# Kernel tuning notes

Measured on AMD Instinct MI355X. Metric: run time of the kernel, lower is better.

The kernel has to match this reference:

```python
import jax, jax.numpy as jnp
import numpy as np

EPS = 0.1

def setup_inputs() -> dict:
    key = jax.random.key(0)
    k1, k2, k3, k4, k5, k6 = jax.random.split(key, 6)
    B, N, Cin, Cout = 8, 2048, 128, 128
    x = jax.random.normal(k1, (B, N, Cin), dtype=jnp.float32)
    x_0 = jax.random.normal(k2, (B, N, Cout), dtype=jnp.float32)
    adj = jax.random.randint(k3, (B, N, N), 0, 2, dtype=jnp.int32)
    # learned parameters (Linear without bias stores weight [out,in]; we keep [in,out])
    W_lin = jax.random.normal(k4, (Cin, Cout), dtype=jnp.float32) / np.sqrt(Cin)
    w_att_l = jax.random.normal(k5, (Cout,), dtype=jnp.float32) / np.sqrt(Cout)
    w_att_r = jax.random.normal(k6, (Cout,), dtype=jnp.float32) / np.sqrt(Cout)
    return {"x": x, "x_0": x_0, "adj": adj, "W_lin": W_lin, "w_att_l": w_att_l, "w_att_r": w_att_r}

def reference(x, x_0, adj, W_lin, w_att_l, w_att_r):
    # x: [B,N,Cin] -> h: [B,N,Cout]
    h = jnp.einsum('bni,io->bno', x, W_lin)
    alpha_l = jnp.einsum('bno,o->bn', h, w_att_l)  # [B,N]
    alpha_r = jnp.einsum('bno,o->bn', h, w_att_r)  # [B,N]
    # alpha[b,i,j] = tanh(alpha_r[b,i] * alpha_l[b,j])
    alpha = jnp.tanh(alpha_r[:, :, None] * alpha_l[:, None, :])  # [B,N,N]
    alpha = jnp.where(adj == 0, jnp.float32(0.0), alpha)
    # dropout p=0.0 -> identity
    out = jnp.einsum('bij,bjo->bio', alpha, h)  # [B,N,Cout]
    return out + EPS * x_0
```

## Files before the change

### kernel.cpp

```cpp
#include <hip/hip_runtime.h>
#include <stdint.h>

#define B_   8
#define N_   2048
#define C_   128
#define EPS_ 0.1f

typedef __attribute__((ext_vector_type(8))) short short8;
typedef __attribute__((ext_vector_type(4))) float f32x4;

__device__ __forceinline__ unsigned short f2bf(float f) {
    union { float f; uint32_t u; } v; v.f = f;
    uint32_t u = v.u + 0x7FFF + ((v.u >> 16) & 1);
    return (unsigned short)(u >> 16);
}

__global__ __launch_bounds__(128) void k_wt(const float* __restrict__ W,
                                            unsigned short* __restrict__ Wt) {
    const int o = blockIdx.x, k = threadIdx.x;
    Wt[o * C_ + k] = f2bf(W[k * C_ + o]);
}

__global__ __launch_bounds__(256) void k_h(
    const float* __restrict__ x, const unsigned short* __restrict__ Wt,
    const float* __restrict__ wl, const float* __restrict__ wr,
    unsigned short* __restrict__ ht, float* __restrict__ al, float* __restrict__ ar)
{
    const int b    = blockIdx.x >> 5;
    const int i0   = (blockIdx.x & 31) * 64;
    const int t    = threadIdx.x;
    const int lane = t & 63;
    const int wid  = t >> 6;

    __shared__ __align__(16) unsigned short xs[64 * 128];
    __shared__ __align__(16) unsigned short ws[128 * 128];

    #pragma unroll
    for (int p = 0; p < 4; ++p) {
        const int s = p * 256 + t, row = s >> 4, u = s & 15;
        const float* gp = x + ((size_t)(b * N_ + i0 + row) * C_ + u * 8);
        float4 f0 = *(const float4*)gp;
        float4 f1 = *(const float4*)(gp + 4);
        short8 tv;
        tv[0] = (short)f2bf(f0.x); tv[1] = (short)f2bf(f0.y);
        tv[2] = (short)f2bf(f0.z); tv[3] = (short)f2bf(f0.w);
        tv[4] = (short)f2bf(f1.x); tv[5] = (short)f2bf(f1.y);
        tv[6] = (short)f2bf(f1.z); tv[7] = (short)f2bf(f1.w);
        *(short8*)&xs[row * 128 + (u ^ (row & 15)) * 8] = tv;
    }
    #pragma unroll
    for (int p = 0; p < 8; ++p) {
        const int s = p * 256 + t, o = s >> 4, u = s & 15;
        int4 v = *(const int4*)(Wt + o * C_ + u * 8);
        *(int4*)&ws[o * 128 + (u ^ (o & 15)) * 8] = v;
    }
    __syncthreads();

    const int m0 = wid * 16, lr = lane & 15, q = lane >> 4;
    f32x4 acc[8];
    #pragma unroll
    for (int i = 0; i < 8; ++i) acc[i] = (f32x4){0.f, 0.f, 0.f, 0.f};

    #pragma unroll
    for (int s = 0; s < 4; ++s) {
        const int m = m0 + lr;
        short8 af = *(const short8*)&xs[m * 128 + ((s * 4 + q) ^ (m & 15)) * 8];
        #pragma unroll
        for (int tt = 0; tt < 8; ++tt) {
            const int o = tt * 16 + lr;
            short8 bf = *(const short8*)&ws[o * 128 + ((s * 4 + q) ^ (o & 15)) * 8];
            acc[tt] = __builtin_amdgcn_mfma_f32_16x16x32_bf16(af, bf, acc[tt], 0, 0, 0);
        }
    }

    float pl[4] = {0.f, 0.f, 0.f, 0.f}, pr[4] = {0.f, 0.f, 0.f, 0.f};
    const int j0 = i0 + m0 + q * 4;
    #pragma unroll
    for (int tt = 0; tt < 8; ++tt) {
        const int o = tt * 16 + lr;
        const float wlv = wl[o], wrv = wr[o];
        unsigned int lo = (unsigned int)f2bf(acc[tt][0]) | ((unsigned int)f2bf(acc[tt][1]) << 16);
        unsigned int hi = (unsigned int)f2bf(acc[tt][2]) | ((unsigned int)f2bf(acc[tt][3]) << 16);
        uint2 u2; u2.x = lo; u2.y = hi;
        *(uint2*)&ht[((size_t)(b * C_ + o)) * N_ + j0] = u2;
        #pragma unroll
        for (int r = 0; r < 4; ++r) {
            pl[r] = fmaf(acc[tt][r], wlv, pl[r]);
            pr[r] = fmaf(acc[tt][r], wrv, pr[r]);
        }
    }
    #pragma unroll
    for (int msk = 1; msk < 16; msk <<= 1) {
        #pragma unroll
        for (int r = 0; r < 4; ++r) {
            pl[r] += __shfl_xor(pl[r], msk, 64);
            pr[r] += __shfl_xor(pr[r], msk, 64);
        }
    }
    if (lr == 0) {
        #pragma unroll
        for (int r = 0; r < 4; ++r) {
            al[b * N_ + j0 + r] = pl[r];
            ar[b * N_ + j0 + r] = pr[r];
        }
    }
}

struct Pref {
    int4   a[4];
    float4 l[4];
    int4   hb[8];
};

__global__ __launch_bounds__(256) void k_out(
    const int* __restrict__ adj, const unsigned short* __restrict__ ht,
    const float* __restrict__ al, const float* __restrict__ ar,
    const float* __restrict__ x0, float* __restrict__ out)
{
    const int b    = blockIdx.x >> 6;
    const int i0   = (blockIdx.x & 63) * 32;
    const int t    = threadIdx.x;
    const int lane = t & 63;
    const int wid  = t >> 6;

    const int m0 = (wid & 1) * 16, n0 = (wid >> 1) * 64;
    const int lr = lane & 15, q = lane >> 4;
    const int q8 = q * 8;

    const int irow = i0 + m0 + lr;
    const float arv = ar[b * N_ + irow];
    const float tl  = 2.f * arv;
    const int*            adjp = adj + ((size_t)(b * N_) + irow) * N_;
    const float*          alp  = al + b * N_;
    const unsigned short* hbp  = ht + ((size_t)(b * C_) + n0 + lr) * N_;

    auto ldc = [&](int c) -> Pref {
        Pref P;
        const int j0 = c * 64 + q8;
        #pragma unroll
        for (int s2 = 0; s2 < 2; ++s2) {
            P.a[s2 * 2]     = *(const int4*)(adjp + j0 + s2 * 32);
            P.a[s2 * 2 + 1] = *(const int4*)(adjp + j0 + s2 * 32 + 4);
            P.l[s2 * 2]     = *(const float4*)(alp + j0 + s2 * 32);
            P.l[s2 * 2 + 1] = *(const float4*)(alp + j0 + s2 * 32 + 4);
            #pragma unroll
            for (int tt = 0; tt < 4; ++tt)
                P.hb[s2 * 4 + tt] =
                    *(const int4*)(hbp + (size_t)(tt * 16) * N_ + j0 + s2 * 32);
        }
        return P;
    };

    f32x4 acc[4];
    #pragma unroll
    for (int i = 0; i < 4; ++i) acc[i] = (f32x4){0.f, 0.f, 0.f, 0.f};

    auto cmp = [&](const Pref& P) {
        #pragma unroll
        for (int s2 = 0; s2 < 2; ++s2) {
            const int*   av = (const int*)&P.a[s2 * 2];
            const float* lv = (const float*)&P.l[s2 * 2];
            short8 af;
            #pragma unroll
            for (int e = 0; e < 8; ++e) {
                float ex = __expf(tl * lv[e]);
                float th = 1.f - 2.f / (ex + 1.f);
                af[e] = av[e] ? (short)f2bf(th) : (short)0;
            }
            #pragma unroll
            for (int tt = 0; tt < 4; ++tt) {
                short8 bf = *(const short8*)&P.hb[s2 * 4 + tt];
                acc[tt] = __builtin_amdgcn_mfma_f32_16x16x32_bf16(af, bf, acc[tt], 0, 0, 0);
            }
        }
    };

    Pref PA = ldc(0);
    #pragma unroll 1
    for (int c = 0; c < 32; c += 2) {
        Pref PB = ldc(c + 1);
        cmp(PA);
        if (c + 2 < 32) PA = ldc(c + 2);
        cmp(PB);
    }

    #pragma unroll
    for (int tt = 0; tt < 4; ++tt) {
        const int o = n0 + tt * 16 + lr;
        #pragma unroll
        for (int r = 0; r < 4; ++r) {
            const int row = i0 + m0 + q * 4 + r;
            const size_t idx = ((size_t)(b * N_) + row) * C_ + o;
            out[idx] = acc[tt][r] + EPS_ * x0[idx];
        }
    }
}

extern "C" void kernel_launch(void* const* d_in, const int* in_sizes, int n_in,
                              void* d_out, int out_size, void* d_ws, size_t ws_size,
                              hipStream_t stream) {
    const float* x   = (const float*)d_in[0];
    const float* x0  = (const float*)d_in[1];
    const int*   adj = (const int*)d_in[2];
    const float* W   = (const float*)d_in[3];
    const float* wl  = (const float*)d_in[4];
    const float* wr  = (const float*)d_in[5];
    float* out = (float*)d_out;

    unsigned short* ht = (unsigned short*)d_ws;
    float* al = (float*)((char*)d_ws + (size_t)B_ * C_ * N_ * 2);
    float* ar = al + B_ * N_;
    unsigned short* Wt = (unsigned short*)(ar + B_ * N_);

    k_wt <<<C_,             C_,  0, stream>>>(W, Wt);
    k_h  <<<B_ * (N_ / 64), 256, 0, stream>>>(x, Wt, wl, wr, ht, al, ar);
    k_out<<<B_ * (N_ / 32), 256, 0, stream>>>(adj, ht, al, ar, x0, out);
}
```

Before: 270.3 us.

## Split k_out over the reduction dimension with LDS cross-wave sum

```diff
diff --git a/kernel.cpp b/kernel.cpp
--- a/kernel.cpp
+++ b/kernel.cpp
@@ -106,94 +106,89 @@
     }
 }
 
-struct Pref {
-    int4   a[4];
-    float4 l[4];
-    int4   hb[8];
-};
-
 __global__ __launch_bounds__(256) void k_out(
     const int* __restrict__ adj, const unsigned short* __restrict__ ht,
     const float* __restrict__ al, const float* __restrict__ ar,
     const float* __restrict__ x0, float* __restrict__ out)
 {
-    const int b    = blockIdx.x >> 6;
-    const int i0   = (blockIdx.x & 63) * 32;
+    const int b    = blockIdx.x & 7;
+    const int i0   = (blockIdx.x >> 3) * 16;
     const int t    = threadIdx.x;
     const int lane = t & 63;
     const int wid  = t >> 6;
-
-    const int m0 = (wid & 1) * 16, n0 = (wid >> 1) * 64;
-    const int lr = lane & 15, q = lane >> 4;
-    const int q8 = q * 8;
-
-    const int irow = i0 + m0 + lr;
-    const float arv = ar[b * N_ + irow];
+    const int lr   = lane & 15, q = lane >> 4;
+
+    __shared__ __align__(16) float red[4][16][132];
+
+    const float arv = ar[b * N_ + i0 + lr];
     const float tl  = 2.f * arv;
-    const int*            adjp = adj + ((size_t)(b * N_) + irow) * N_;
-    const float*          alp  = al + b * N_;
-    const unsigned short* hbp  = ht + ((size_t)(b * C_) + n0 + lr) * N_;
-
-    auto ldc = [&](int c) -> Pref {
-        Pref P;
-        const int j0 = c * 64 + q8;
+
+    const int*            adjp = adj + ((size_t)(b * N_) + i0 + lr) * N_ + q * 8;
+    const float*          alp  = al + b * N_ + q * 8;
+    const unsigned short* htp  = ht + ((size_t)(b * C_) + lr) * N_ + q * 8;
+
+    f32x4 acc[8];
+    #pragma unroll
+    for (int i = 0; i < 8; ++i) acc[i] = (f32x4){0.f, 0.f, 0.f, 0.f};
+
+    #pragma unroll 1
+    for (int k = 0; k < 8; ++k) {
+        const int j0 = (wid * 8 + k) * 64;
         #pragma unroll
         for (int s2 = 0; s2 < 2; ++s2) {
-            P.a[s2 * 2]     = *(const int4*)(adjp + j0 + s2 * 32);
-            P.a[s2 * 2 + 1] = *(const int4*)(adjp + j0 + s2 * 32 + 4);
-            P.l[s2 * 2]     = *(const float4*)(alp + j0 + s2 * 32);
-            P.l[s2 * 2 + 1] = *(const float4*)(alp + j0 + s2 * 32 + 4);
-            #pragma unroll
-            for (int tt = 0; tt < 4; ++tt)
-                P.hb[s2 * 4 + tt] =
-                    *(const int4*)(hbp + (size_t)(tt * 16) * N_ + j0 + s2 * 32);
-        }
-        return P;
-    };
-
-    f32x4 acc[4];
-    #pragma unroll
-    for (int i = 0; i < 4; ++i) acc[i] = (f32x4){0.f, 0.f, 0.f, 0.f};
-
-    auto cmp = [&](const Pref& P) {
-        #pragma unroll
-        for (int s2 = 0; s2 < 2; ++s2) {
-            const int*   av = (const int*)&P.a[s2 * 2];
-            const float* lv = (const float*)&P.l[s2 * 2];
+            const int jo = j0 + s2 * 32;
+            int4 a01[2];
+            a01[0] = *(const int4*)(adjp + jo);
+            a01[1] = *(const int4*)(adjp + jo + 4);
+            float4 l01[2];
+            l01[0] = *(const float4*)(alp + jo);
+            l01[1] = *(const float4*)(alp + jo + 4);
+            const int*   av = (const int*)a01;
+            const float* lv = (const float*)l01;
             short8 af;
             #pragma unroll
             for (int e = 0; e < 8; ++e) {
                 float ex = __expf(tl * lv[e]);
-                float th = 1.f - 2.f / (ex + 1.f);
+                float th = 1.f - 2.f * __builtin_amdgcn_rcpf(ex + 1.f);
                 af[e] = av[e] ? (short)f2bf(th) : (short)0;
             }
             #pragma unroll
-            for (int tt = 0; tt < 4; ++tt) {
-                short8 bf = *(const short8*)&P.hb[s2 * 4 + tt];
+            for (int tt = 0; tt < 8; ++tt) {
+                short8 bf = *(const short8*)(htp + (size_t)(tt * 16) * N_ + jo);
                 acc[tt] = __builtin_amdgcn_mfma_f32_16x16x32_bf16(af, bf, acc[tt], 0, 0, 0);
             }
         }
-    };
-
-    Pref PA = ldc(0);
-    #pragma unroll 1
-    for (int c = 0; c < 32; c += 2) {
-        Pref PB = ldc(c + 1);
-        cmp(PA);
-        if (c + 2 < 32) PA = ldc(c + 2);
-        cmp(PB);
-    }
-
-    #pragma unroll
-    for (int tt = 0; tt < 4; ++tt) {
-        const int o = n0 + tt * 16 + lr;
-        #pragma unroll
-        for (int r = 0; r < 4; ++r) {
-            const int row = i0 + m0 + q * 4 + r;
-            const size_t idx = ((size_t)(b * N_) + row) * C_ + o;
-            out[idx] = acc[tt][r] + EPS_ * x0[idx];
-        }
-    }
+    }
+
+    #pragma unroll
+    for (int tt = 0; tt < 8; ++tt)
+        #pragma unroll
+        for (int r = 0; r < 4; ++r)
+            red[wid][q * 4 + r][tt * 16 + lr] = acc[tt][r];
+    __syncthreads();
+
+    const int row = t >> 4;
+    const int c0  = (t & 15) * 8;
+    float s[8];
+    #pragma unroll
+    for (int e = 0; e < 8; ++e) s[e] = 0.f;
+    #pragma unroll
+    for (int w = 0; w < 4; ++w) {
+        float4 v0 = *(const float4*)&red[w][row][c0];
+        float4 v1 = *(const float4*)&red[w][row][c0 + 4];
+        s[0] += v0.x; s[1] += v0.y; s[2] += v0.z; s[3] += v0.w;
+        s[4] += v1.x; s[5] += v1.y; s[6] += v1.z; s[7] += v1.w;
+    }
+    const size_t idx = ((size_t)(b * N_) + i0 + row) * C_ + c0;
+    float4 xa = *(const float4*)(x0 + idx);
+    float4 xb = *(const float4*)(x0 + idx + 4);
+    float4 o0, o1;
+    o0.x = s[0] + EPS_ * xa.x; o0.y = s[1] + EPS_ * xa.y;
+    o0.z = s[2] + EPS_ * xa.z; o0.w = s[3] + EPS_ * xa.w;
+    o1.x = s[4] + EPS_ * xb.x; o1.y = s[5] + EPS_ * xb.y;
+    o1.z = s[6] + EPS_ * xb.z; o1.w = s[7] + EPS_ * xb.w;
+    *(float4*)(out + idx)     = o0;
+    *(float4*)(out + idx + 4) = o1;
 }
 
 extern "C" void kernel_launch(void* const* d_in, const int* in_sizes, int n_in,
@@ -214,5 +209,5 @@
 
     k_wt <<<C_,             C_,  0, stream>>>(W, Wt);
     k_h  <<<B_ * (N_ / 64), 256, 0, stream>>>(x, Wt, wl, wr, ht, al, ar);
-    k_out<<<B_ * (N_ / 32), 256, 0, stream>>>(adj, ht, al, ar, x0, out);
-}
+    k_out<<<B_ * (N_ / 16), 256, 0, stream>>>(adj, ht, al, ar, x0, out);
+}
```

Measured after the change: 275.0 us. No clear change (+1.7%).
